# Optimization experiments

Hardware: AMD Instinct MI355X
Metric: run time of the kernel (lower is better)

## Reference

```python
import jax, jax.numpy as jnp
import numpy as np

BN_EPS = 1e-5
NN_EPS = 1e-8
K = 3


def conv_bn_relu(x, W, b, gamma, beta, mean, var):
    # x: [B, Cin, N]; W: [Cout, Cin] (1x1 conv); BN in inference mode w/ running stats
    y = jnp.einsum('bcn,oc->bon', x, W) + b[None, :, None]
    y = (y - mean[None, :, None]) * (gamma / jnp.sqrt(var + BN_EPS))[None, :, None] + beta[None, :, None]
    return jax.nn.relu(y)


def three_interpolation(p1, p2, f2):
    # p1: [B, N1, 3] unknown xyz; p2: [B, N2, 3] known xyz; f2: [B, C, N2]
    # squared pairwise distances via the expansion trick (avoids [B,N1,N2,3])
    d2 = (jnp.sum(p1 * p1, -1)[:, :, None]
          + jnp.sum(p2 * p2, -1)[:, None, :]
          - 2.0 * jnp.einsum('bnd,bmd->bnm', p1, p2))  # [B, N1, N2]
    neg_d2, idx = jax.lax.top_k(-d2, K)                 # 3 nearest
    dist = -neg_d2                                      # squared dists, [B, N1, 3]
    recip = 1.0 / (dist + NN_EPS)
    weight = recip / jnp.sum(recip, axis=-1, keepdims=True)  # [B, N1, 3]
    f2t = jnp.transpose(f2, (0, 2, 1))                  # [B, N2, C]
    gathered = jax.vmap(lambda f, i: f[i])(f2t, idx)    # [B, N1, 3, C]
    return jnp.einsum('bnkc,bnk->bcn', gathered, weight)  # [B, C, N1]


def setup_inputs() -> dict:
    key = jax.random.key(0)
    ks = jax.random.split(key, 16)
    B, N1, N2 = 8, 16384, 4096
    mlp = [256, 128, 128]
    inp = {
        'p1': jax.random.normal(ks[0], (B, N1, 3), jnp.float32),
        'p2': jax.random.normal(ks[1], (B, N2, 3), jnp.float32),
        'f2': jax.random.normal(ks[2], (B, mlp[0], N2), jnp.float32),
    }
    kidx = 3
    for li in range(len(mlp) - 1):
        cin, cout = mlp[li], mlp[li + 1]
        inp[f'W{li}'] = jax.random.normal(ks[kidx], (cout, cin), jnp.float32) * (1.0 / np.sqrt(cin)); kidx += 1
        inp[f'b{li}'] = jnp.zeros((cout,), jnp.float32)
        inp[f'gamma{li}'] = jnp.ones((cout,), jnp.float32)
        inp[f'beta{li}'] = jnp.zeros((cout,), jnp.float32)
        inp[f'mean{li}'] = jax.random.normal(ks[kidx], (cout,), jnp.float32) * 0.1; kidx += 1
        inp[f'var{li}'] = jax.random.uniform(ks[kidx], (cout,), jnp.float32, 0.5, 1.5); kidx += 1
    return inp


def reference(p1, p2, f2,
              W0, b0, gamma0, beta0, mean0, var0,
              W1, b1, gamma1, beta1, mean1, var1):
    f = conv_bn_relu(f2, W0, b0, gamma0, beta0, mean0, var0)
    f = conv_bn_relu(f, W1, b1, gamma1, beta1, mean1, var1)
    return three_interpolation(p1, p2, f)
```

## Files before the change

kernel.cpp:

```cpp
#include <hip/hip_runtime.h>

#define B_    8
#define N1_   16384
#define N2_   4096
#define NTOT_ (B_ * N1_)

__device__ __forceinline__ float np_sumsq(float x, float y, float z)
{
#pragma clang fp contract(off)
    return ((x * x + y * y) + z * z);
}

__global__ __launch_bounds__(256) void fold_kernel(
    const float* __restrict__ W, const float* __restrict__ bias,
    const float* __restrict__ gamma, const float* __restrict__ beta,
    const float* __restrict__ mean, const float* __restrict__ var,
    float* __restrict__ Wp, float* __restrict__ bp, int Cout, int Cin)
{
    int t = blockIdx.x * 256 + threadIdx.x;
    if (t < Cout * Cin) {
        int o = t / Cin;
        float s = gamma[o] / sqrtf(var[o] + 1e-5f);
        Wp[t] = W[t] * s;
    }
    if (t < Cout) {
        float s = gamma[t] / sqrtf(var[t] + 1e-5f);
        bp[t] = beta[t] + (bias[t] - mean[t]) * s;
    }
}

__global__ __launch_bounds__(256) void q4_kernel(
    const float* __restrict__ p2, float4* __restrict__ q4)
{
    int t = blockIdx.x * 256 + threadIdx.x;
    float x = p2[3 * (size_t)t + 0];
    float y = p2[3 * (size_t)t + 1];
    float z = p2[3 * (size_t)t + 2];
    q4[t] = make_float4(x, y, z, np_sumsq(x, y, z));
}

template <int CIN, bool TRANS>
__global__ __launch_bounds__(256) void gemm_relu_kernel(
    const float* __restrict__ X, const float* __restrict__ Wp,
    const float* __restrict__ bp, float* __restrict__ Y)
{
    __shared__ float A_lds[32][136];
    __shared__ float B_lds[32][128];

    const int b  = blockIdx.y;
    const int n0 = blockIdx.x * 128;
    const int tid = threadIdx.x;
    const int ty = tid >> 4;
    const int tx = tid & 15;
    const float* Xb = X + (size_t)b * CIN * N2_;

    float acc[8][8];
#pragma unroll
    for (int i = 0; i < 8; ++i)
#pragma unroll
        for (int j = 0; j < 8; ++j) acc[i][j] = 0.f;

    const int a_kq = (tid & 7) * 4;
    const int a_r0 = tid >> 3;
    const int b_n4 = (tid & 31) * 4;
    const int b_k0 = tid >> 5;

    for (int k0 = 0; k0 < CIN; k0 += 32) {
#pragma unroll
        for (int i = 0; i < 4; ++i) {
            const int row = a_r0 + 32 * i;
            const float4 v = *(const float4*)&Wp[(size_t)row * CIN + k0 + a_kq];
            A_lds[a_kq + 0][row] = v.x;
            A_lds[a_kq + 1][row] = v.y;
            A_lds[a_kq + 2][row] = v.z;
            A_lds[a_kq + 3][row] = v.w;
        }
#pragma unroll
        for (int i = 0; i < 4; ++i) {
            const int krow = b_k0 + 8 * i;
            *(float4*)&B_lds[krow][b_n4] =
                *(const float4*)&Xb[(size_t)(k0 + krow) * N2_ + n0 + b_n4];
        }
        __syncthreads();

#pragma unroll
        for (int kk = 0; kk < 32; ++kk) {
            const float4 a0 = *(const float4*)&A_lds[kk][ty * 4];
            const float4 a1 = *(const float4*)&A_lds[kk][64 + ty * 4];
            const float4 bq0 = *(const float4*)&B_lds[kk][tx * 4];
            const float4 bq1 = *(const float4*)&B_lds[kk][64 + tx * 4];
            const float av[8] = {a0.x, a0.y, a0.z, a0.w, a1.x, a1.y, a1.z, a1.w};
            const float bv[8] = {bq0.x, bq0.y, bq0.z, bq0.w, bq1.x, bq1.y, bq1.z, bq1.w};
#pragma unroll
            for (int i = 0; i < 8; ++i)
#pragma unroll
                for (int j = 0; j < 8; ++j)
                    acc[i][j] = fmaf(av[i], bv[j], acc[i][j]);
        }
        __syncthreads();
    }

    float bias_v[8];
#pragma unroll
    for (int i = 0; i < 8; ++i) {
        const int r = (i < 4) ? (ty * 4 + i) : (64 + ty * 4 + (i - 4));
        bias_v[i] = bp[r];
    }

    if (!TRANS) {
#pragma unroll
        for (int i = 0; i < 8; ++i) {
            const int r = (i < 4) ? (ty * 4 + i) : (64 + ty * 4 + (i - 4));
            float* yrow = Y + ((size_t)b * 128 + r) * N2_ + n0;
            float4 v0, v1;
            v0.x = fmaxf(acc[i][0] + bias_v[i], 0.f);
            v0.y = fmaxf(acc[i][1] + bias_v[i], 0.f);
            v0.z = fmaxf(acc[i][2] + bias_v[i], 0.f);
            v0.w = fmaxf(acc[i][3] + bias_v[i], 0.f);
            v1.x = fmaxf(acc[i][4] + bias_v[i], 0.f);
            v1.y = fmaxf(acc[i][5] + bias_v[i], 0.f);
            v1.z = fmaxf(acc[i][6] + bias_v[i], 0.f);
            v1.w = fmaxf(acc[i][7] + bias_v[i], 0.f);
            *(float4*)(yrow + tx * 4) = v0;
            *(float4*)(yrow + 64 + tx * 4) = v1;
        }
    } else {
        float (*T)[132] = (float(*)[132])&A_lds[0][0];
#pragma unroll
        for (int s = 0; s < 4; ++s) {
            if ((tx >> 3) == (s & 1)) {
                const int joff = (s >> 1) * 4;
                const int cl0 = (tx & 7) * 4;
#pragma unroll
                for (int i = 0; i < 8; ++i) {
                    const int r = (i < 4) ? (ty * 4 + i) : (64 + ty * 4 + (i - 4));
#pragma unroll
                    for (int j = 0; j < 4; ++j)
                        T[cl0 + j][r] = fmaxf(acc[i][j + joff] + bias_v[i], 0.f);
                }
            }
            __syncthreads();
#pragma unroll
            for (int p = 0; p < 4; ++p) {
                const int row = (tid >> 5) + 8 * p;
                const float4 v = *(const float4*)&T[row][(tid & 31) * 4];
                float* orow = Y + ((size_t)b * N2_ + n0 + 32 * s + row) * 128;
                *(float4*)&orow[(tid & 31) * 4] = v;
            }
            __syncthreads();
        }
    }
}

__global__ __launch_bounds__(256, 8) void knn_phase1(
    const float* __restrict__ p1, const float4* __restrict__ q4,
    float* __restrict__ part_d, int* __restrict__ part_i)
{
    __shared__ float4 qs[1024];
    const int tid = threadIdx.x;
    const int chunk = blockIdx.x & 3;
    const int g = (blockIdx.x >> 2) * 256 + tid;
    const int b = g >> 14;

    const float px = p1[3 * (size_t)g + 0];
    const float py = p1[3 * (size_t)g + 1];
    const float pz = p1[3 * (size_t)g + 2];
    const float s1 = np_sumsq(px, py, pz);

    const float4* qb = q4 + (size_t)b * N2_ + chunk * 1024;
#pragma unroll
    for (int i = 0; i < 4; ++i) qs[tid + i * 256] = qb[tid + i * 256];
    __syncthreads();

    float d0 = 1e30f, d1 = 1e30f, d2v = 1e30f;
    int i0 = 0, i1 = 0, i2 = 0;
    const int jbase = chunk * 1024;

    for (int j = 0; j < 1024; j += 4) {
#pragma unroll
        for (int u = 0; u < 4; ++u) {
            const float4 q = qs[j + u];
            const float dot = __fmaf_rn(px, q.x, __fmaf_rn(py, q.y, __fmul_rn(pz, q.z)));
            const float ss  = s1 + q.w;
            const float t   = __fmaf_rn(-2.0f, dot, ss);
            if (t < d2v) {
                const int jj = jbase + j + u;
                const bool c1 = t < d1, c0 = t < d0;
                d2v = c1 ? d1 : t;                 i2 = c1 ? i1 : jj;
                const float nd1 = c1 ? (c0 ? d0 : t) : d1;
                const int   ni1 = c1 ? (c0 ? i0 : jj) : i1;
                d1 = nd1;                          i1 = ni1;
                d0 = c0 ? t : d0;                  i0 = c0 ? jj : i0;
            }
        }
    }

    part_d[(0 * 4 + chunk) * NTOT_ + g] = d0;
    part_d[(1 * 4 + chunk) * NTOT_ + g] = d1;
    part_d[(2 * 4 + chunk) * NTOT_ + g] = d2v;
    part_i[(0 * 4 + chunk) * NTOT_ + g] = i0;
    part_i[(1 * 4 + chunk) * NTOT_ + g] = i1;
    part_i[(2 * 4 + chunk) * NTOT_ + g] = i2;
}

__global__ __launch_bounds__(256) void knn_merge(
    const float* __restrict__ part_d, const int* __restrict__ part_i,
    int* __restrict__ idx_ws, float* __restrict__ w_ws)
{
    const int g = blockIdx.x * 256 + threadIdx.x;

    float d0 = 1e30f, d1 = 1e30f, d2v = 1e30f;
    int i0 = 0, i1 = 0, i2 = 0;

#pragma unroll
    for (int c = 0; c < 4; ++c) {
#pragma unroll
        for (int k = 0; k < 3; ++k) {
            const float t = part_d[(k * 4 + c) * NTOT_ + g];
            const int  jj = part_i[(k * 4 + c) * NTOT_ + g];
            if (t < d2v) {
                const bool c1 = t < d1, c0 = t < d0;
                d2v = c1 ? d1 : t;                 i2 = c1 ? i1 : jj;
                const float nd1 = c1 ? (c0 ? d0 : t) : d1;
                const int   ni1 = c1 ? (c0 ? i0 : jj) : i1;
                d1 = nd1;                          i1 = ni1;
                d0 = c0 ? t : d0;                  i0 = c0 ? jj : i0;
            }
        }
    }

    float w0, w1, w2;
    {
#pragma clang fp contract(off)
        const float r0 = 1.0f / (d0 + 1e-8f);
        const float r1 = 1.0f / (d1 + 1e-8f);
        const float r2 = 1.0f / (d2v + 1e-8f);
        const float rs = (r0 + r1) + r2;
        w0 = r0 / rs;
        w1 = r1 / rs;
        w2 = r2 / rs;
    }

    idx_ws[g]             = i0;
    idx_ws[NTOT_ + g]     = i1;
    idx_ws[2 * NTOT_ + g] = i2;
    w_ws[g]               = w0;
    w_ws[NTOT_ + g]       = w1;
    w_ws[2 * NTOT_ + g]   = w2;
}

__global__ __launch_bounds__(256) void gather_kernel(
    const float* __restrict__ f_t, const int* __restrict__ idx_ws,
    const float* __restrict__ w_ws, float* __restrict__ out)
{
    const int tid = threadIdx.x;
    const int lane = tid & 63, cg = tid >> 6;
    const int g = blockIdx.x * 64 + lane;
    const int b = g >> 14, n = g & 16383;

    const int i0 = idx_ws[g];
    const int i1 = idx_ws[NTOT_ + g];
    const int i2 = idx_ws[2 * NTOT_ + g];
    const float w0 = w_ws[g];
    const float w1 = w_ws[NTOT_ + g];
    const float w2 = w_ws[2 * NTOT_ + g];

    const float* base = f_t + (size_t)b * N2_ * 128 + cg * 32;
    const float4* r0 = (const float4*)(base + (size_t)i0 * 128);
    const float4* r1 = (const float4*)(base + (size_t)i1 * 128);
    const float4* r2 = (const float4*)(base + (size_t)i2 * 128);

    float acc[32];
#pragma unroll
    for (int q = 0; q < 8; ++q) {
        const float4 a = r0[q], bb = r1[q], c = r2[q];
        acc[4 * q + 0] = fmaf(w0, a.x, fmaf(w1, bb.x, w2 * c.x));
        acc[4 * q + 1] = fmaf(w0, a.y, fmaf(w1, bb.y, w2 * c.y));
        acc[4 * q + 2] = fmaf(w0, a.z, fmaf(w1, bb.z, w2 * c.z));
        acc[4 * q + 3] = fmaf(w0, a.w, fmaf(w1, bb.w, w2 * c.w));
    }

    float* ob = out + ((size_t)b * 128 + cg * 32) * N1_ + n;
#pragma unroll
    for (int c = 0; c < 32; ++c)
        __builtin_nontemporal_store(acc[c], ob + (size_t)c * N1_);
}

extern "C" void kernel_launch(void* const* d_in, const int* in_sizes, int n_in,
                              void* d_out, int out_size, void* d_ws, size_t ws_size,
                              hipStream_t stream)
{
    const float* p1  = (const float*)d_in[0];
    const float* p2  = (const float*)d_in[1];
    const float* f2  = (const float*)d_in[2];
    const float* W0  = (const float*)d_in[3];
    const float* b0  = (const float*)d_in[4];
    const float* g0  = (const float*)d_in[5];
    const float* be0 = (const float*)d_in[6];
    const float* m0  = (const float*)d_in[7];
    const float* v0  = (const float*)d_in[8];
    const float* W1  = (const float*)d_in[9];
    const float* b1  = (const float*)d_in[10];
    const float* g1  = (const float*)d_in[11];
    const float* be1 = (const float*)d_in[12];
    const float* m1  = (const float*)d_in[13];
    const float* v1  = (const float*)d_in[14];

    char* ws = (char*)d_ws;
    float4* q4  = (float4*)(ws);
    float*  W0p = (float*)(ws + (512 << 10));
    float*  b0p = (float*)(ws + (640 << 10));
    float*  W1p = (float*)(ws + (644 << 10));
    float*  b1p = (float*)(ws + (708 << 10));
    float*  h   = (float*)(ws + ((size_t)1 << 20));
    float*  f_t = (float*)(ws + ((size_t)17 << 20));
    int*    idxw= (int*)  (ws + ((size_t)33 << 20));
    float*  wgt = (float*)(ws + ((size_t)35 << 20));
    float*  pd  = (float*)(ws + ((size_t)1 << 20));
    int*    pi  = (int*)  (ws + ((size_t)9 << 20));

    fold_kernel<<<128, 256, 0, stream>>>(W0, b0, g0, be0, m0, v0, W0p, b0p, 128, 256);
    fold_kernel<<<64, 256, 0, stream>>>(W1, b1, g1, be1, m1, v1, W1p, b1p, 128, 128);
    q4_kernel<<<(B_ * N2_) / 256, 256, 0, stream>>>(p2, q4);

    gemm_relu_kernel<256, false><<<dim3(32, 8), 256, 0, stream>>>(f2, W0p, b0p, h);
    gemm_relu_kernel<128, true ><<<dim3(32, 8), 256, 0, stream>>>(h, W1p, b1p, f_t);

    knn_phase1<<<(NTOT_ / 256) * 4, 256, 0, stream>>>(p1, q4, pd, pi);
    knn_merge<<<NTOT_ / 256, 256, 0, stream>>>(pd, pi, idxw, wgt);
    gather_kernel<<<NTOT_ / 64, 256, 0, stream>>>(f_t, idxw, wgt, (float*)d_out);
}
```

Baseline: 354.5 us.

## Fuse prep kernels, merge kNN merge into gather, halve GEMM N-tile

The two BN-fold kernels and the p2 packing kernel become one prep kernel. The kNN partial merge and weight computation move into the gather kernel, which removes the idx/weight workspace round trip and one launch. Gather blocks are remapped so that consecutive blocks interleave across batches. The 1x1-conv GEMM tile shrinks from 128 to 64 columns, doubling the block count to improve occupancy on the 256-CU GPU, at the cost of less register reuse per thread.

```diff
diff --git a/kernel.cpp b/kernel.cpp
--- a/kernel.cpp
+++ b/kernel.cpp
@@ -11,32 +11,45 @@
     return ((x * x + y * y) + z * z);
 }
 
-__global__ __launch_bounds__(256) void fold_kernel(
-    const float* __restrict__ W, const float* __restrict__ bias,
-    const float* __restrict__ gamma, const float* __restrict__ beta,
-    const float* __restrict__ mean, const float* __restrict__ var,
-    float* __restrict__ Wp, float* __restrict__ bp, int Cout, int Cin)
-{
-    int t = blockIdx.x * 256 + threadIdx.x;
-    if (t < Cout * Cin) {
-        int o = t / Cin;
-        float s = gamma[o] / sqrtf(var[o] + 1e-5f);
-        Wp[t] = W[t] * s;
-    }
-    if (t < Cout) {
-        float s = gamma[t] / sqrtf(var[t] + 1e-5f);
-        bp[t] = beta[t] + (bias[t] - mean[t]) * s;
-    }
-}
-
-__global__ __launch_bounds__(256) void q4_kernel(
-    const float* __restrict__ p2, float4* __restrict__ q4)
-{
-    int t = blockIdx.x * 256 + threadIdx.x;
-    float x = p2[3 * (size_t)t + 0];
-    float y = p2[3 * (size_t)t + 1];
-    float z = p2[3 * (size_t)t + 2];
-    q4[t] = make_float4(x, y, z, np_sumsq(x, y, z));
+__global__ __launch_bounds__(256) void prep_kernel(
+    const float* __restrict__ W0, const float* __restrict__ b0,
+    const float* __restrict__ g0, const float* __restrict__ be0,
+    const float* __restrict__ m0, const float* __restrict__ v0,
+    const float* __restrict__ W1, const float* __restrict__ b1,
+    const float* __restrict__ g1, const float* __restrict__ be1,
+    const float* __restrict__ m1, const float* __restrict__ v1,
+    const float* __restrict__ p2,
+    float* __restrict__ W0p, float* __restrict__ b0p,
+    float* __restrict__ W1p, float* __restrict__ b1p,
+    float4* __restrict__ q4)
+{
+    const int bx = blockIdx.x;
+    const int tid = threadIdx.x;
+    if (bx < 128) {
+        const int t = bx * 256 + tid;
+        const int o = t >> 8;
+        const float s = g0[o] / sqrtf(v0[o] + 1e-5f);
+        W0p[t] = W0[t] * s;
+        if (t < 128) {
+            const float ss = g0[t] / sqrtf(v0[t] + 1e-5f);
+            b0p[t] = be0[t] + (b0[t] - m0[t]) * ss;
+        }
+    } else if (bx < 192) {
+        const int t = (bx - 128) * 256 + tid;
+        const int o = t >> 7;
+        const float s = g1[o] / sqrtf(v1[o] + 1e-5f);
+        W1p[t] = W1[t] * s;
+        if (t < 128) {
+            const float ss = g1[t] / sqrtf(v1[t] + 1e-5f);
+            b1p[t] = be1[t] + (b1[t] - m1[t]) * ss;
+        }
+    } else {
+        const int t = (bx - 192) * 256 + tid;
+        const float x = p2[3 * (size_t)t + 0];
+        const float y = p2[3 * (size_t)t + 1];
+        const float z = p2[3 * (size_t)t + 2];
+        q4[t] = make_float4(x, y, z, np_sumsq(x, y, z));
+    }
 }
 
 template <int CIN, bool TRANS>
@@ -45,25 +58,25 @@
     const float* __restrict__ bp, float* __restrict__ Y)
 {
     __shared__ float A_lds[32][136];
-    __shared__ float B_lds[32][128];
+    __shared__ float B_lds[32][64];
 
     const int b  = blockIdx.y;
-    const int n0 = blockIdx.x * 128;
+    const int n0 = blockIdx.x * 64;
     const int tid = threadIdx.x;
     const int ty = tid >> 4;
     const int tx = tid & 15;
     const float* Xb = X + (size_t)b * CIN * N2_;
 
-    float acc[8][8];
+    float acc[8][4];
 #pragma unroll
     for (int i = 0; i < 8; ++i)
 #pragma unroll
-        for (int j = 0; j < 8; ++j) acc[i][j] = 0.f;
+        for (int j = 0; j < 4; ++j) acc[i][j] = 0.f;
 
     const int a_kq = (tid & 7) * 4;
     const int a_r0 = tid >> 3;
-    const int b_n4 = (tid & 31) * 4;
-    const int b_k0 = tid >> 5;
+    const int b_n4 = (tid & 15) * 4;
+    const int b_k0 = tid >> 4;
 
     for (int k0 = 0; k0 < CIN; k0 += 32) {
 #pragma unroll
@@ -76,8 +89,8 @@
             A_lds[a_kq + 3][row] = v.w;
         }
 #pragma unroll
-        for (int i = 0; i < 4; ++i) {
-            const int krow = b_k0 + 8 * i;
+        for (int i = 0; i < 2; ++i) {
+            const int krow = b_k0 + 16 * i;
             *(float4*)&B_lds[krow][b_n4] =
                 *(const float4*)&Xb[(size_t)(k0 + krow) * N2_ + n0 + b_n4];
         }
@@ -87,14 +100,13 @@
         for (int kk = 0; kk < 32; ++kk) {
             const float4 a0 = *(const float4*)&A_lds[kk][ty * 4];
             const float4 a1 = *(const float4*)&A_lds[kk][64 + ty * 4];
-            const float4 bq0 = *(const float4*)&B_lds[kk][tx * 4];
-            const float4 bq1 = *(const float4*)&B_lds[kk][64 + tx * 4];
+            const float4 bq = *(const float4*)&B_lds[kk][tx * 4];
             const float av[8] = {a0.x, a0.y, a0.z, a0.w, a1.x, a1.y, a1.z, a1.w};
-            const float bv[8] = {bq0.x, bq0.y, bq0.z, bq0.w, bq1.x, bq1.y, bq1.z, bq1.w};
+            const float bv[4] = {bq.x, bq.y, bq.z, bq.w};
 #pragma unroll
             for (int i = 0; i < 8; ++i)
 #pragma unroll
-                for (int j = 0; j < 8; ++j)
+                for (int j = 0; j < 4; ++j)
                     acc[i][j] = fmaf(av[i], bv[j], acc[i][j]);
         }
         __syncthreads();
@@ -112,31 +124,25 @@
         for (int i = 0; i < 8; ++i) {
             const int r = (i < 4) ? (ty * 4 + i) : (64 + ty * 4 + (i - 4));
             float* yrow = Y + ((size_t)b * 128 + r) * N2_ + n0;
-            float4 v0, v1;
+            float4 v0;
             v0.x = fmaxf(acc[i][0] + bias_v[i], 0.f);
             v0.y = fmaxf(acc[i][1] + bias_v[i], 0.f);
             v0.z = fmaxf(acc[i][2] + bias_v[i], 0.f);
             v0.w = fmaxf(acc[i][3] + bias_v[i], 0.f);
-            v1.x = fmaxf(acc[i][4] + bias_v[i], 0.f);
-            v1.y = fmaxf(acc[i][5] + bias_v[i], 0.f);
-            v1.z = fmaxf(acc[i][6] + bias_v[i], 0.f);
-            v1.w = fmaxf(acc[i][7] + bias_v[i], 0.f);
             *(float4*)(yrow + tx * 4) = v0;
-            *(float4*)(yrow + 64 + tx * 4) = v1;
         }
     } else {
         float (*T)[132] = (float(*)[132])&A_lds[0][0];
 #pragma unroll
-        for (int s = 0; s < 4; ++s) {
-            if ((tx >> 3) == (s & 1)) {
-                const int joff = (s >> 1) * 4;
+        for (int s = 0; s < 2; ++s) {
+            if ((tx >> 3) == s) {
                 const int cl0 = (tx & 7) * 4;
 #pragma unroll
                 for (int i = 0; i < 8; ++i) {
                     const int r = (i < 4) ? (ty * 4 + i) : (64 + ty * 4 + (i - 4));
 #pragma unroll
                     for (int j = 0; j < 4; ++j)
-                        T[cl0 + j][r] = fmaxf(acc[i][j + joff] + bias_v[i], 0.f);
+                        T[cl0 + j][r] = fmaxf(acc[i][j] + bias_v[i], 0.f);
                 }
             }
             __syncthreads();
@@ -203,15 +209,18 @@
     part_i[(2 * 4 + chunk) * NTOT_ + g] = i2;
 }
 
-__global__ __launch_bounds__(256) void knn_merge(
-    const float* __restrict__ part_d, const int* __restrict__ part_i,
-    int* __restrict__ idx_ws, float* __restrict__ w_ws)
-{
-    const int g = blockIdx.x * 256 + threadIdx.x;
+__global__ __launch_bounds__(256) void gather_kernel(
+    const float* __restrict__ f_t, const float* __restrict__ part_d,
+    const int* __restrict__ part_i, float* __restrict__ out)
+{
+    const int tid = threadIdx.x;
+    const int lane = tid & 63, cg = tid >> 6;
+    const int vb = (blockIdx.x & 7) * 256 + (blockIdx.x >> 3);
+    const int g = vb * 64 + lane;
+    const int b = g >> 14, n = g & 16383;
 
     float d0 = 1e30f, d1 = 1e30f, d2v = 1e30f;
     int i0 = 0, i1 = 0, i2 = 0;
-
 #pragma unroll
     for (int c = 0; c < 4; ++c) {
 #pragma unroll
@@ -241,39 +250,15 @@
         w2 = r2 / rs;
     }
 
-    idx_ws[g]             = i0;
-    idx_ws[NTOT_ + g]     = i1;
-    idx_ws[2 * NTOT_ + g] = i2;
-    w_ws[g]               = w0;
-    w_ws[NTOT_ + g]       = w1;
-    w_ws[2 * NTOT_ + g]   = w2;
-}
-
-__global__ __launch_bounds__(256) void gather_kernel(
-    const float* __restrict__ f_t, const int* __restrict__ idx_ws,
-    const float* __restrict__ w_ws, float* __restrict__ out)
-{
-    const int tid = threadIdx.x;
-    const int lane = tid & 63, cg = tid >> 6;
-    const int g = blockIdx.x * 64 + lane;
-    const int b = g >> 14, n = g & 16383;
-
-    const int i0 = idx_ws[g];
-    const int i1 = idx_ws[NTOT_ + g];
-    const int i2 = idx_ws[2 * NTOT_ + g];
-    const float w0 = w_ws[g];
-    const float w1 = w_ws[NTOT_ + g];
-    const float w2 = w_ws[2 * NTOT_ + g];
-
     const float* base = f_t + (size_t)b * N2_ * 128 + cg * 32;
-    const float4* r0 = (const float4*)(base + (size_t)i0 * 128);
-    const float4* r1 = (const float4*)(base + (size_t)i1 * 128);
-    const float4* r2 = (const float4*)(base + (size_t)i2 * 128);
+    const float4* r0v = (const float4*)(base + (size_t)i0 * 128);
+    const float4* r1v = (const float4*)(base + (size_t)i1 * 128);
+    const float4* r2v = (const float4*)(base + (size_t)i2 * 128);
 
     float acc[32];
 #pragma unroll
     for (int q = 0; q < 8; ++q) {
-        const float4 a = r0[q], bb = r1[q], c = r2[q];
+        const float4 a = r0v[q], bb = r1v[q], c = r2v[q];
         acc[4 * q + 0] = fmaf(w0, a.x, fmaf(w1, bb.x, w2 * c.x));
         acc[4 * q + 1] = fmaf(w0, a.y, fmaf(w1, bb.y, w2 * c.y));
         acc[4 * q + 2] = fmaf(w0, a.z, fmaf(w1, bb.z, w2 * c.z));
@@ -314,19 +299,16 @@
     float*  b1p = (float*)(ws + (708 << 10));
     float*  h   = (float*)(ws + ((size_t)1 << 20));
     float*  f_t = (float*)(ws + ((size_t)17 << 20));
-    int*    idxw= (int*)  (ws + ((size_t)33 << 20));
-    float*  wgt = (float*)(ws + ((size_t)35 << 20));
     float*  pd  = (float*)(ws + ((size_t)1 << 20));
     int*    pi  = (int*)  (ws + ((size_t)9 << 20));
 
-    fold_kernel<<<128, 256, 0, stream>>>(W0, b0, g0, be0, m0, v0, W0p, b0p, 128, 256);
-    fold_kernel<<<64, 256, 0, stream>>>(W1, b1, g1, be1, m1, v1, W1p, b1p, 128, 128);
-    q4_kernel<<<(B_ * N2_) / 256, 256, 0, stream>>>(p2, q4);
-
-    gemm_relu_kernel<256, false><<<dim3(32, 8), 256, 0, stream>>>(f2, W0p, b0p, h);
-    gemm_relu_kernel<128, true ><<<dim3(32, 8), 256, 0, stream>>>(h, W1p, b1p, f_t);
+    prep_kernel<<<320, 256, 0, stream>>>(W0, b0, g0, be0, m0, v0,
+                                         W1, b1, g1, be1, m1, v1,
+                                         p2, W0p, b0p, W1p, b1p, q4);
+
+    gemm_relu_kernel<256, false><<<dim3(64, 8), 256, 0, stream>>>(f2, W0p, b0p, h);
+    gemm_relu_kernel<128, true ><<<dim3(64, 8), 256, 0, stream>>>(h, W1p, b1p, f_t);
 
     knn_phase1<<<(NTOT_ / 256) * 4, 256, 0, stream>>>(p1, q4, pd, pi);
-    knn_merge<<<NTOT_ / 256, 256, 0, stream>>>(pd, pi, idxw, wgt);
-    gather_kernel<<<NTOT_ / 64, 256, 0, stream>>>(f_t, idxw, wgt, (float*)d_out);
-}
+    gather_kernel<<<NTOT_ / 64, 256, 0, stream>>>(f_t, pd, pi, (float*)d_out);
+}
```

Result: no change. 354.4 us (-0.0%).
